# Performance work log

Measured on AMD Instinct MI355X. Metric: run time of the kernel, lower is better.

## Reference

```python
import jax, jax.numpy as jnp
import numpy as np

TOPK = 3
RAT_S = 0.05


def _zero_window_mask(h, w, rat_s=RAT_S):
    # mask[src_pixel, tgt_r, tgt_c] = 1 - gauss_r * gauss_c, gaussian centered at src pixel
    sr = h * rat_s
    sc = w * rat_s
    rows = jnp.arange(h, dtype=jnp.float32)
    cols = jnp.arange(w, dtype=jnp.float32)
    gr = jnp.exp(-((rows[None, :] - rows[:, None]) ** 2) / (2.0 * sr * sr))  # (h_src, h_tgt)
    gc = jnp.exp(-((cols[None, :] - cols[:, None]) ** 2) / (2.0 * sc * sc))  # (w_src, w_tgt)
    mask = 1.0 - gr[:, None, :, None] * gc[None, :, None, :]                 # (h,w,h,w)
    return mask.reshape(h * w, h * w)


def setup_inputs() -> dict:
    key = jax.random.key(0)
    b, c, h, w = 2, 256, 64, 64
    x = jax.random.normal(key, (b, c, h, w), dtype=jnp.float32)
    alpha = jnp.float32(5.0)
    return {"x": x, "alpha": alpha}


def reference(x, alpha):
    b, c, h, w = x.shape
    hw = h * w
    # L2-normalize over channels (F.normalize eps=1e-12 uses max(norm, eps))
    nrm = jnp.sqrt(jnp.sum(x * x, axis=1, keepdims=True))
    xn = x / jnp.maximum(nrm, 1e-12)
    xf = xn.reshape(b, c, hw)
    # (b, hw_src, hw_tgt) affinity
    aff = jnp.einsum('bcs,bct->bst', xf, xf)
    mask = _zero_window_mask(h, w)
    x_aff = aff * mask[None]                               # (b, hw, hw)
    logits = x_aff * alpha
    x_c = jax.nn.softmax(logits, axis=-1) * jax.nn.softmax(logits, axis=-2)
    xc_o = x_c.reshape(b, hw, h, w)
    # top-k over source-pixel axis (dim=-3)
    val = jax.lax.top_k(jnp.moveaxis(xc_o, 1, -1), TOPK)[0]  # (b,h,w,k)
    val = jnp.moveaxis(val, -1, 1)                           # (b,k,h,w)
    x_soft = xc_o / (jnp.sum(xc_o, axis=1, keepdims=True) + 1e-8)
    return (val, x_soft)
```

## Files before the change

### kernel.cpp

```cpp
#include <hip/hip_runtime.h>

#define HW 4096
#define CDIM 256
#define BK 32

typedef _Float16 half8 __attribute__((ext_vector_type(8)));
typedef _Float16 half4v __attribute__((ext_vector_type(4)));
typedef float f32x4 __attribute__((ext_vector_type(4)));

__device__ __forceinline__ void top3_ins(float v, float& a0, float& a1, float& a2) {
  float m01 = fminf(a0, v);
  a0 = fmaxf(a0, v);
  float m12 = fminf(a1, m01);
  a1 = fmaxf(a1, m01);
  a2 = fmaxf(a2, m12);
}

__device__ __forceinline__ float mask_val(const float* gtab, int s, int t) {
  int dr = (s >> 6) - (t >> 6); dr = dr < 0 ? -dr : dr;
  int dc = (s & 63) - (t & 63); dc = dc < 0 ? -dc : dc;
  return 1.0f - gtab[dr] * gtab[dc];
}

__device__ __forceinline__ void async_copy16(const void* g, void* l) {
  __builtin_amdgcn_global_load_lds((const __attribute__((address_space(1))) void*)g,
                                   (__attribute__((address_space(3))) void*)l, 16, 0, 0);
}

__device__ __forceinline__ void stage_slice(const _Float16* __restrict__ X,
                                            int rowBase, int k0,
                                            _Float16* sdst, int w, int lane) {
  const int csrc = ((lane & 3) - ((lane >> 3) & 3)) & 3;
#pragma unroll
  for (int i = 0; i < 2; ++i) {
    const int rchunk = w * 32 + i * 16;
    const _Float16* g =
        X + (size_t)(rowBase + rchunk + (lane >> 2)) * CDIM + k0 + csrc * 8;
    async_copy16(g, sdst + rchunk * BK);
  }
}

__global__ void __launch_bounds__(256) normalize_k(const float* __restrict__ x,
                                                   _Float16* __restrict__ Xf) {
  const int p = threadIdx.x & 31;
  const int g = threadIdx.x >> 5;
  const int P0 = blockIdx.x * 32;
  const int b = P0 >> 12;
  const int ph = (P0 & (HW - 1)) + p;
  const float* xb = x + (size_t)b * CDIM * HW + ph;
  float vals[32];
  float ss = 0.f;
#pragma unroll
  for (int k = 0; k < 32; ++k) {
    float v = xb[(size_t)(g * 32 + k) * HW];
    vals[k] = v;
    ss += v * v;
  }
  __shared__ float ssqp[8][33];
  __shared__ float scl[32];
  ssqp[g][p] = ss;
  __syncthreads();
  if (threadIdx.x < 32) {
    float s2 = 0.f;
#pragma unroll
    for (int gg = 0; gg < 8; ++gg) s2 += ssqp[gg][threadIdx.x];
    scl[threadIdx.x] = 1.0f / fmaxf(sqrtf(s2), 1e-12f);
  }
  __syncthreads();
  const float sc = scl[p];
  _Float16* o = Xf + (size_t)(P0 + p) * CDIM + g * 32;
#pragma unroll
  for (int c8 = 0; c8 < 4; ++c8) {
    half8 h;
#pragma unroll
    for (int j = 0; j < 8; ++j) h[j] = (_Float16)(vals[c8 * 8 + j] * sc);
    *(half8*)(o + c8 * 8) = h;
  }
}

__global__ void __launch_bounds__(256, 3) gemmE16_k(const _Float16* __restrict__ Xf,
                                                    const float* __restrict__ alphap,
                                                    float* __restrict__ R,
                                                    float* __restrict__ outX) {
  __shared__ _Float16 sA[2][128 * BK];
  __shared__ _Float16 sB[2][128 * BK];
  __shared__ float gtab[64];
  if (threadIdx.x < 64) {
    float d = (float)threadIdx.x;
    gtab[threadIdx.x] = __expf(-d * d * 0.048828125f);
  }
  const float alpha = alphap[0];
  const int b = blockIdx.z;
  const _Float16* X = Xf + (size_t)b * HW * CDIM;
  const int lane = threadIdx.x & 63;
  const int w = threadIdx.x >> 6;
  const int wr = w >> 1, wc = w & 1;
  const int mBase = blockIdx.y * 128;
  const int nBase = blockIdx.x * 128;

  f32x4 acc[4][4];
#pragma unroll
  for (int mi = 0; mi < 4; ++mi)
#pragma unroll
    for (int ni = 0; ni < 4; ++ni) acc[mi][ni] = (f32x4){0.f, 0.f, 0.f, 0.f};

  const int aRow0 = wr * 64 + (lane & 15);
  const int bRow0 = wc * 64 + (lane & 15);
  const int cswz = (((lane >> 4) + ((lane >> 1) & 3)) & 3) * 8;

  stage_slice(X, mBase, 0, sA[0], w, lane);
  stage_slice(X, nBase, 0, sB[0], w, lane);

  int cur = 0;
#pragma unroll
  for (int k0 = 0; k0 < CDIM; k0 += BK) {
    __syncthreads();
    if (k0 + BK < CDIM) {
      stage_slice(X, mBase, k0 + BK, sA[cur ^ 1], w, lane);
      stage_slice(X, nBase, k0 + BK, sB[cur ^ 1], w, lane);
    }
    half8 a[4], bfr[4];
#pragma unroll
    for (int i = 0; i < 4; ++i)
      a[i] = *(const half8*)(sA[cur] + (aRow0 + 16 * i) * BK + cswz);
#pragma unroll
    for (int i = 0; i < 4; ++i)
      bfr[i] = *(const half8*)(sB[cur] + (bRow0 + 16 * i) * BK + cswz);
#pragma unroll
    for (int mi = 0; mi < 4; ++mi)
#pragma unroll
      for (int ni = 0; ni < 4; ++ni)
        acc[mi][ni] = __builtin_amdgcn_mfma_f32_16x16x32_f16(a[mi], bfr[ni], acc[mi][ni], 0, 0, 0);
    cur ^= 1;
  }

  const int quad = lane >> 4;
  _Float16* Hb = (_Float16*)(outX + (size_t)b * HW * HW);
  float csum[4] = {0.f, 0.f, 0.f, 0.f};
#pragma unroll
  for (int mi = 0; mi < 4; ++mi) {
#pragma unroll
    for (int r = 0; r < 4; ++r) {
      const int s = mBase + wr * 64 + mi * 16 + quad * 4 + r;
      _Float16* hrow = Hb + (size_t)s * (2 * HW);
#pragma unroll
      for (int ni = 0; ni < 4; ++ni) {
        const int t = nBase + wc * 64 + ni * 16 + (lane & 15);
        float e = __expf(alpha * mask_val(gtab, s, t) * acc[mi][ni][r]);
        csum[ni] += e;
        hrow[t] = (_Float16)e;
      }
    }
  }
#pragma unroll
  for (int off = 16; off < 64; off <<= 1)
#pragma unroll
    for (int ni = 0; ni < 4; ++ni) csum[ni] += __shfl_xor(csum[ni], off);
  if (quad == 0) {
#pragma unroll
    for (int ni = 0; ni < 4; ++ni)
      atomicAdd(&R[b * HW + nBase + wc * 64 + ni * 16 + (lane & 15)], csum[ni]);
  }
}

__global__ void __launch_bounds__(256) colstats16_k(const float* __restrict__ outX,
                                                    const float* __restrict__ R,
                                                    float* __restrict__ T,
                                                    float* __restrict__ part) {
  const int b = blockIdx.z;
  const _Float16* Hb = (const _Float16*)(outX + (size_t)b * HW * HW);
  const float* Rb = R + b * HW;
  const int s0 = blockIdx.x * 1024;
  const int t0 = blockIdx.y * 64;
  const int tg = threadIdx.x & 15;
  const int sr = threadIdx.x >> 4;
  float ts[4] = {0.f, 0.f, 0.f, 0.f};
  float q0[4] = {0.f, 0.f, 0.f, 0.f}, q1[4] = {0.f, 0.f, 0.f, 0.f}, q2[4] = {0.f, 0.f, 0.f, 0.f};
#pragma unroll 4
  for (int k = 0; k < 64; ++k) {
    const int s = s0 + k * 16 + sr;
    const float inv = 1.0f / Rb[s];
    half4v ev = *(const half4v*)(Hb + (size_t)s * (2 * HW) + t0 + tg * 4);
#pragma unroll
    for (int j = 0; j < 4; ++j) {
      float e = (float)ev[j];
      float gval = e * e * inv;
      ts[j] += gval;
      top3_ins(gval, q0[j], q1[j], q2[j]);
    }
  }
  __shared__ float Tp[16][68], P0a[16][68], P1a[16][68], P2a[16][68];
#pragma unroll
  for (int j = 0; j < 4; ++j) {
    Tp[sr][tg * 4 + j] = ts[j];
    P0a[sr][tg * 4 + j] = q0[j];
    P1a[sr][tg * 4 + j] = q1[j];
    P2a[sr][tg * 4 + j] = q2[j];
  }
  __syncthreads();
  if (threadIdx.x < 64) {
    float tsum = 0.f, a0 = 0.f, a1 = 0.f, a2 = 0.f;
#pragma unroll
    for (int s2 = 0; s2 < 16; ++s2) {
      tsum += Tp[s2][threadIdx.x];
      top3_ins(P0a[s2][threadIdx.x], a0, a1, a2);
      top3_ins(P1a[s2][threadIdx.x], a0, a1, a2);
      top3_ins(P2a[s2][threadIdx.x], a0, a1, a2);
    }
    const int t = t0 + threadIdx.x;
    atomicAdd(&T[b * HW + t], tsum);
    float* pp = part + ((size_t)(b * 4 + blockIdx.x) * HW + t) * 3;
    pp[0] = a0;
    pp[1] = a1;
    pp[2] = a2;
  }
}

__global__ void __launch_bounds__(256) merge_k(const float* __restrict__ R,
                                               const float* __restrict__ T,
                                               const float* __restrict__ part,
                                               float* __restrict__ W,
                                               float* __restrict__ val_out) {
  const int idx = blockIdx.x * 256 + threadIdx.x;
  const int b = idx >> 12;
  const int t = idx & (HW - 1);
  float a0 = 0.f, a1 = 0.f, a2 = 0.f;
#pragma unroll
  for (int c = 0; c < 4; ++c) {
    const float* pp = part + ((size_t)(b * 4 + c) * HW + t) * 3;
    top3_ins(pp[0], a0, a1, a2);
    top3_ins(pp[1], a0, a1, a2);
    top3_ins(pp[2], a0, a1, a2);
  }
  const float r = R[idx];
  const float invr = 1.0f / r;
  val_out[(b * 3 + 0) * HW + t] = a0 * invr;
  val_out[(b * 3 + 1) * HW + t] = a1 * invr;
  val_out[(b * 3 + 2) * HW + t] = a2 * invr;
  W[idx] = 1.0f / (T[idx] + 1e-8f * r);
}

#define WROWS 8
__global__ void __launch_bounds__(256) writeout16_k(const float* __restrict__ R,
                                                    const float* __restrict__ W,
                                                    float* __restrict__ X) {
  const int b = blockIdx.y;
  float* Xb = X + (size_t)b * HW * HW;
  const _Float16* Hb = (const _Float16*)Xb;
  const float* Wb = W + b * HW;
  const float* Rb = R + b * HW;
  const int s0 = blockIdx.x * WROWS;
  f32x4 wv[4];
#pragma unroll
  for (int it = 0; it < 4; ++it)
    wv[it] = *(const f32x4*)(Wb + it * 1024 + threadIdx.x * 4);
  half4v ehA[4], ehB[4];
#pragma unroll
  for (int it = 0; it < 4; ++it)
    ehA[it] = *(const half4v*)(Hb + (size_t)s0 * (2 * HW) + it * 1024 + threadIdx.x * 4);
#pragma unroll
  for (int row = 0; row < WROWS; ++row) {
    __syncthreads();
    if (row + 1 < WROWS) {
      const _Float16* hn = Hb + (size_t)(s0 + row + 1) * (2 * HW);
#pragma unroll
      for (int it = 0; it < 4; ++it) {
        half4v v = *(const half4v*)(hn + it * 1024 + threadIdx.x * 4);
        if (row & 1) ehA[it] = v; else ehB[it] = v;
      }
    }
    const float inv = 1.0f / Rb[s0 + row];
    float* rowp = Xb + (size_t)(s0 + row) * HW;
#pragma unroll
    for (int it = 0; it < 4; ++it) {
      const int t = it * 1024 + threadIdx.x * 4;
      half4v cur = (row & 1) ? ehB[it] : ehA[it];
      f32x4 o;
#pragma unroll
      for (int j = 0; j < 4; ++j) {
        float e = (float)cur[j];
        o[j] = e * e * inv * wv[it][j];
      }
      *(f32x4*)(rowp + t) = o;
    }
  }
}

extern "C" void kernel_launch(void* const* d_in, const int* in_sizes, int n_in,
                              void* d_out, int out_size, void* d_ws, size_t ws_size,
                              hipStream_t stream) {
  const float* x = (const float*)d_in[0];
  const float* alphap = (const float*)d_in[1];
  float* out = (float*)d_out;
  float* out_val = out;
  float* out_x = out + 2 * 3 * HW;
  char* ws = (char*)d_ws;

  _Float16* Xf = (_Float16*)ws;
  float* R = (float*)(ws + (size_t)4194304);
  float* T = R + 2 * HW;
  float* W = T + 2 * HW;
  float* part = W + 2 * HW;

  hipMemsetAsync(R, 0, (size_t)2 * HW * 2 * sizeof(float), stream);

  normalize_k<<<dim3(256), dim3(256), 0, stream>>>(x, Xf);
  gemmE16_k<<<dim3(32, 32, 2), dim3(256), 0, stream>>>(Xf, alphap, R, out_x);
  colstats16_k<<<dim3(4, 64, 2), dim3(256), 0, stream>>>(out_x, R, T, part);
  merge_k<<<dim3(32), dim3(256), 0, stream>>>(R, T, part, W, out_val);
  writeout16_k<<<dim3(512, 2), dim3(256), 0, stream>>>(R, W, out_x);
}
```

Baseline: 203.8 us.

## Stage GEMM epilogue tile through LDS for coalesced 16-byte stores; widen colstats loads

The GEMM epilogue now writes exp values into a swizzled LDS tile that reuses the operand buffers, then stores each row with coalesced half8 (16-byte) writes instead of scattered 2-byte stores. The column-stats kernel reads 8 halves per thread instead of 4, with 32 row groups per block. The aim is to cut uncoalesced global write and read transactions on the large intermediate. It adds two block barriers and more shared memory and registers in colstats, which may lower occupancy.

```diff
diff --git a/kernel.cpp b/kernel.cpp
--- a/kernel.cpp
+++ b/kernel.cpp
@@ -5,7 +5,6 @@
 #define BK 32
 
 typedef _Float16 half8 __attribute__((ext_vector_type(8)));
-typedef _Float16 half4v __attribute__((ext_vector_type(4)));
 typedef float f32x4 __attribute__((ext_vector_type(4)));
 
 __device__ __forceinline__ void top3_ins(float v, float& a0, float& a1, float& a2) {
@@ -82,8 +81,7 @@
                                                     const float* __restrict__ alphap,
                                                     float* __restrict__ R,
                                                     float* __restrict__ outX) {
-  __shared__ _Float16 sA[2][128 * BK];
-  __shared__ _Float16 sB[2][128 * BK];
+  __shared__ _Float16 smem[4][128 * BK];
   __shared__ float gtab[64];
   if (threadIdx.x < 64) {
     float d = (float)threadIdx.x;
@@ -108,24 +106,24 @@
   const int bRow0 = wc * 64 + (lane & 15);
   const int cswz = (((lane >> 4) + ((lane >> 1) & 3)) & 3) * 8;
 
-  stage_slice(X, mBase, 0, sA[0], w, lane);
-  stage_slice(X, nBase, 0, sB[0], w, lane);
+  stage_slice(X, mBase, 0, smem[0], w, lane);
+  stage_slice(X, nBase, 0, smem[2], w, lane);
 
   int cur = 0;
 #pragma unroll
   for (int k0 = 0; k0 < CDIM; k0 += BK) {
     __syncthreads();
     if (k0 + BK < CDIM) {
-      stage_slice(X, mBase, k0 + BK, sA[cur ^ 1], w, lane);
-      stage_slice(X, nBase, k0 + BK, sB[cur ^ 1], w, lane);
+      stage_slice(X, mBase, k0 + BK, smem[cur ^ 1], w, lane);
+      stage_slice(X, nBase, k0 + BK, smem[2 + (cur ^ 1)], w, lane);
     }
     half8 a[4], bfr[4];
 #pragma unroll
     for (int i = 0; i < 4; ++i)
-      a[i] = *(const half8*)(sA[cur] + (aRow0 + 16 * i) * BK + cswz);
+      a[i] = *(const half8*)(smem[cur] + (aRow0 + 16 * i) * BK + cswz);
 #pragma unroll
     for (int i = 0; i < 4; ++i)
-      bfr[i] = *(const half8*)(sB[cur] + (bRow0 + 16 * i) * BK + cswz);
+      bfr[i] = *(const half8*)(smem[2 + cur] + (bRow0 + 16 * i) * BK + cswz);
 #pragma unroll
     for (int mi = 0; mi < 4; ++mi)
 #pragma unroll
@@ -134,21 +132,24 @@
     cur ^= 1;
   }
 
+  __syncthreads();
+  _Float16* et = &smem[0][0];
   const int quad = lane >> 4;
-  _Float16* Hb = (_Float16*)(outX + (size_t)b * HW * HW);
   float csum[4] = {0.f, 0.f, 0.f, 0.f};
 #pragma unroll
   for (int mi = 0; mi < 4; ++mi) {
 #pragma unroll
     for (int r = 0; r < 4; ++r) {
-      const int s = mBase + wr * 64 + mi * 16 + quad * 4 + r;
-      _Float16* hrow = Hb + (size_t)s * (2 * HW);
+      const int row = wr * 64 + mi * 16 + quad * 4 + r;
+      const int s = mBase + row;
+      const int v = (row >> 2) & 7;
 #pragma unroll
       for (int ni = 0; ni < 4; ++ni) {
-        const int t = nBase + wc * 64 + ni * 16 + (lane & 15);
+        const int col = wc * 64 + ni * 16 + (lane & 15);
+        const int t = nBase + col;
         float e = __expf(alpha * mask_val(gtab, s, t) * acc[mi][ni][r]);
         csum[ni] += e;
-        hrow[t] = (_Float16)e;
+        et[row * 128 + ((((col >> 4) ^ v) << 4) | (col & 15))] = (_Float16)e;
       }
     }
   }
@@ -160,6 +161,17 @@
 #pragma unroll
     for (int ni = 0; ni < 4; ++ni)
       atomicAdd(&R[b * HW + nBase + wc * 64 + ni * 16 + (lane & 15)], csum[ni]);
+  }
+  __syncthreads();
+  _Float16* Hb = (_Float16*)(outX + (size_t)b * HW * HW);
+  const int c8 = threadIdx.x & 15;
+  const int r0 = threadIdx.x >> 4;
+#pragma unroll
+  for (int pass = 0; pass < 8; ++pass) {
+    const int row = pass * 16 + r0;
+    const int v = (row >> 2) & 7;
+    half8 hv = *(const half8*)(et + row * 128 + ((((c8 >> 1) ^ v) << 4) | ((c8 & 1) * 8)));
+    *(half8*)(Hb + (size_t)(mBase + row) * (2 * HW) + nBase + c8 * 8) = hv;
   }
 }
 
@@ -172,36 +184,37 @@
   const float* Rb = R + b * HW;
   const int s0 = blockIdx.x * 1024;
   const int t0 = blockIdx.y * 64;
-  const int tg = threadIdx.x & 15;
-  const int sr = threadIdx.x >> 4;
-  float ts[4] = {0.f, 0.f, 0.f, 0.f};
-  float q0[4] = {0.f, 0.f, 0.f, 0.f}, q1[4] = {0.f, 0.f, 0.f, 0.f}, q2[4] = {0.f, 0.f, 0.f, 0.f};
+  const int tg = threadIdx.x & 7;
+  const int sr = threadIdx.x >> 3;
+  float ts[8], q0[8], q1[8], q2[8];
+#pragma unroll
+  for (int j = 0; j < 8; ++j) { ts[j] = 0.f; q0[j] = 0.f; q1[j] = 0.f; q2[j] = 0.f; }
 #pragma unroll 4
-  for (int k = 0; k < 64; ++k) {
-    const int s = s0 + k * 16 + sr;
+  for (int k = 0; k < 32; ++k) {
+    const int s = s0 + k * 32 + sr;
     const float inv = 1.0f / Rb[s];
-    half4v ev = *(const half4v*)(Hb + (size_t)s * (2 * HW) + t0 + tg * 4);
-#pragma unroll
-    for (int j = 0; j < 4; ++j) {
+    half8 ev = *(const half8*)(Hb + (size_t)s * (2 * HW) + t0 + tg * 8);
+#pragma unroll
+    for (int j = 0; j < 8; ++j) {
       float e = (float)ev[j];
       float gval = e * e * inv;
       ts[j] += gval;
       top3_ins(gval, q0[j], q1[j], q2[j]);
     }
   }
-  __shared__ float Tp[16][68], P0a[16][68], P1a[16][68], P2a[16][68];
-#pragma unroll
-  for (int j = 0; j < 4; ++j) {
-    Tp[sr][tg * 4 + j] = ts[j];
-    P0a[sr][tg * 4 + j] = q0[j];
-    P1a[sr][tg * 4 + j] = q1[j];
-    P2a[sr][tg * 4 + j] = q2[j];
+  __shared__ float Tp[32][68], P0a[32][68], P1a[32][68], P2a[32][68];
+#pragma unroll
+  for (int j = 0; j < 8; ++j) {
+    Tp[sr][tg * 8 + j] = ts[j];
+    P0a[sr][tg * 8 + j] = q0[j];
+    P1a[sr][tg * 8 + j] = q1[j];
+    P2a[sr][tg * 8 + j] = q2[j];
   }
   __syncthreads();
   if (threadIdx.x < 64) {
     float tsum = 0.f, a0 = 0.f, a1 = 0.f, a2 = 0.f;
 #pragma unroll
-    for (int s2 = 0; s2 < 16; ++s2) {
+    for (int s2 = 0; s2 < 32; ++s2) {
       tsum += Tp[s2][threadIdx.x];
       top3_ins(P0a[s2][threadIdx.x], a0, a1, a2);
       top3_ins(P1a[s2][threadIdx.x], a0, a1, a2);
@@ -241,6 +254,7 @@
 }
 
 #define WROWS 8
+typedef _Float16 half4v __attribute__((ext_vector_type(4)));
 __global__ void __launch_bounds__(256) writeout16_k(const float* __restrict__ R,
                                                     const float* __restrict__ W,
                                                     float* __restrict__ X) {
```

New measurement: 204.6 us. No clear change (+0.4%).
